# Performance work log

Hardware: AMD Instinct MI355X
Metric: run time of the kernel (lower is better)

## Reference

```python
import jax, jax.numpy as jnp
import numpy as np

N = 50000
E = 400000
IN_FEATS = 256
HIDDEN = 64
HEADS = 8
CLASSES = 40
NEG_SLOPE = 0.2  # DGL GATConv default negative_slope


def setup_inputs() -> dict:
    key = jax.random.key(0)
    ks = jax.random.split(key, 12)
    features = jax.random.normal(ks[0], (N, IN_FEATS), dtype=jnp.float32)
    src = jax.random.randint(ks[1], (E,), 0, N, dtype=jnp.int32)
    dst = jax.random.randint(ks[2], (E,), 0, N, dtype=jnp.int32)
    s = 0.05
    # layer 0: in_feats -> HEADS*HIDDEN
    W1 = jax.random.normal(ks[3], (IN_FEATS, HEADS * HIDDEN), dtype=jnp.float32) * s
    al1 = jax.random.normal(ks[4], (HEADS, HIDDEN), dtype=jnp.float32) * s
    ar1 = jax.random.normal(ks[5], (HEADS, HIDDEN), dtype=jnp.float32) * s
    # layer 1: HEADS*HIDDEN -> HEADS*HIDDEN
    W2 = jax.random.normal(ks[6], (HEADS * HIDDEN, HEADS * HIDDEN), dtype=jnp.float32) * s
    al2 = jax.random.normal(ks[7], (HEADS, HIDDEN), dtype=jnp.float32) * s
    ar2 = jax.random.normal(ks[8], (HEADS, HIDDEN), dtype=jnp.float32) * s
    # layer 2: HEADS*HIDDEN -> 1*CLASSES
    W3 = jax.random.normal(ks[9], (HEADS * HIDDEN, CLASSES), dtype=jnp.float32) * s
    al3 = jax.random.normal(ks[10], (1, CLASSES), dtype=jnp.float32) * s
    ar3 = jax.random.normal(ks[11], (1, CLASSES), dtype=jnp.float32) * s
    return {"features": features, "src": src, "dst": dst,
            "W1": W1, "al1": al1, "ar1": ar1,
            "W2": W2, "al2": al2, "ar2": ar2,
            "W3": W3, "al3": al3, "ar3": ar3}


def gat_conv(h, W, al, ar, src, dst):
    """DGL GATConv (no bias, no residual, no activation, no dropout)."""
    H, D = al.shape
    feat = (h @ W).reshape(N, H, D)                      # [N,H,D]
    el = jnp.sum(feat * al[None], axis=-1)               # [N,H]
    er = jnp.sum(feat * ar[None], axis=-1)               # [N,H]
    e = jax.nn.leaky_relu(el[src] + er[dst], NEG_SLOPE)  # [E,H]
    # edge softmax over incoming edges of each dst node
    m = jax.ops.segment_max(e, dst, num_segments=N)      # [N,H]
    ex = jnp.exp(e - m[dst])                             # [E,H]
    denom = jax.ops.segment_sum(ex, dst, num_segments=N) # [N,H]
    alpha = ex / denom[dst]                              # [E,H]
    msg = alpha[:, :, None] * feat[src]                  # [E,H,D]
    out = jax.ops.segment_sum(msg, dst, num_segments=N)  # [N,H,D]
    return out.reshape(N, H * D)


def reference(features, src, dst, W1, al1, ar1, W2, al2, ar2, W3, al3, ar3):
    h = gat_conv(features, W1, al1, ar1, src, dst)  # [N, HEADS*HIDDEN]
    h = gat_conv(h, W2, al2, ar2, src, dst)         # [N, HEADS*HIDDEN]
    h = gat_conv(h, W3, al3, ar3, src, dst)         # [N, CLASSES]
    return h
```

## Files before the change

### kernel.cpp

```cpp
#include <hip/hip_runtime.h>
#include <hip/hip_bf16.h>

#define NN 50000
#define NE 400000
#define MPAD 50048
#define SLOTS 48

typedef __bf16 bf16x8_t __attribute__((ext_vector_type(8)));
typedef __bf16 bf16x4_t __attribute__((ext_vector_type(4)));
typedef float f32x4_t __attribute__((ext_vector_type(4)));

__device__ __forceinline__ float bhi(unsigned int u) {
    union { unsigned int i; float f; } v; v.i = u & 0xffff0000u; return v.f;
}
__device__ __forceinline__ float blo(unsigned int u) {
    union { unsigned int i; float f; } v; v.i = u << 16; return v.f;
}

__global__ __launch_bounds__(256) void prep_kernel(
    const float* __restrict__ W1, __hip_bfloat16* __restrict__ W1t,
    const float* __restrict__ W2, __hip_bfloat16* __restrict__ W2t,
    const float* __restrict__ W3, __hip_bfloat16* __restrict__ W3t,
    const float* __restrict__ al1, const float* __restrict__ ar1,
    const float* __restrict__ al2, const float* __restrict__ ar2,
    __hip_bfloat16* __restrict__ walr1, __hip_bfloat16* __restrict__ walr2) {
    int stride = gridDim.x * blockDim.x;
    for (int i = blockIdx.x * blockDim.x + threadIdx.x; i < 512 * 512; i += stride) {
        if (i < 512 * 256) {
            int n = i >> 8, k = i & 255;
            W1t[i] = __float2bfloat16(W1[k * 512 + n]);
        }
        {
            int n = i >> 9, k = i & 511;
            W2t[i] = __float2bfloat16(W2[k * 512 + n]);
        }
        if (i < 48 * 512) {
            int n = i >> 9, k = i & 511;
            W3t[i] = __float2bfloat16((n < 40) ? W3[k * 40 + n] : 0.f);
        }
        if (i < 16 * 256) {
            int j = i >> 8, k = i & 255;
            const float* v = (j < 8) ? (al1 + j * 64) : (ar1 + (j - 8) * 64);
            float s = 0.f;
            for (int d = 0; d < 64; ++d) s += W1[(size_t)k * 512 + (j & 7) * 64 + d] * v[d];
            walr1[(k >> 5) * 512 + j * 32 + (k & 31)] = __float2bfloat16(s);
        }
        if (i < 16 * 512) {
            int j = i >> 9, k = i & 511;
            const float* v = (j < 8) ? (al2 + j * 64) : (ar2 + (j - 8) * 64);
            float s = 0.f;
            for (int d = 0; d < 64; ++d) s += W2[(size_t)k * 512 + (j & 7) * 64 + d] * v[d];
            walr2[(k >> 5) * 512 + j * 32 + (k & 31)] = __float2bfloat16(s);
        }
    }
}

__global__ void build_kernel(const int* __restrict__ src, const int* __restrict__ dst,
                             int* __restrict__ deg, int* __restrict__ slot) {
    int e = blockIdx.x * blockDim.x + threadIdx.x;
    if (e < NE) {
        int d = dst[e];
        int p = atomicAdd(&deg[d], 1);
        if (p < SLOTS) slot[(size_t)d * SLOTS + p] = src[e];
    }
}

__device__ __forceinline__ void gld_lds16(const void* g, void* l) {
    __builtin_amdgcn_global_load_lds(
        (const __attribute__((address_space(1))) unsigned int*)g,
        (__attribute__((address_space(3))) unsigned int*)l, 16, 0, 0);
}

__global__ __launch_bounds__(256) void gemm1_fused(const float* __restrict__ A,
                                                   const __hip_bfloat16* __restrict__ Wt,
                                                   const __hip_bfloat16* __restrict__ walr,
                                                   __hip_bfloat16* __restrict__ C,
                                                   float* __restrict__ el,
                                                   float* __restrict__ er) {
    const int K = 256;
    __shared__ __align__(16) char smem[16384];
    char* smemA = smem;
    char* smemB = smem + 8192;
    const int row0 = blockIdx.x * 128;
    const int col0 = blockIdx.y * 128;
    const int w = threadIdx.x >> 6;
    const int lane = threadIdx.x & 63;
    const int quad = lane >> 4, l15 = lane & 15;
    const int wm = (w >> 1) * 64, wn = (w & 1) * 64;
    const int c0 = w * 2;
    const int srow = lane >> 2;
    const int skel = (lane & 3) * 8;
    const bool my_e = (blockIdx.y == 0) && ((w & 1) == 0);

    f32x4_t acc[4][4] = {};
    f32x4_t acce[4] = {};
    for (int k0 = 0; k0 < K; k0 += 32) {
        __syncthreads();
        {
#pragma unroll
            for (int cc = 0; cc < 2; ++cc) {
                int row = row0 + (c0 + cc) * 16 + srow;
                int rc = (row < NN) ? row : (NN - 1);
                const float* p = A + (size_t)rc * K + k0 + skel;
                float4 f0 = *reinterpret_cast<const float4*>(p);
                float4 f1 = *reinterpret_cast<const float4*>(p + 4);
                bf16x8_t h;
                h[0] = (__bf16)f0.x; h[1] = (__bf16)f0.y;
                h[2] = (__bf16)f0.z; h[3] = (__bf16)f0.w;
                h[4] = (__bf16)f1.x; h[5] = (__bf16)f1.y;
                h[6] = (__bf16)f1.z; h[7] = (__bf16)f1.w;
                *reinterpret_cast<bf16x8_t*>(smemA + (c0 + cc) * 1024 + srow * 64 +
                                             (lane & 3) * 16) = h;
            }
            const __hip_bfloat16* gB0 = Wt + (size_t)(col0 + c0 * 16 + srow) * K + k0 + skel;
            gld_lds16(gB0, smemB + c0 * 1024);
            gld_lds16(gB0 + (size_t)16 * K, smemB + (c0 + 1) * 1024);
        }
        __syncthreads();
        bf16x8_t a[4], b[4];
#pragma unroll
        for (int mi = 0; mi < 4; mi++)
            a[mi] = *reinterpret_cast<const bf16x8_t*>(smemA + (wm + mi * 16 + l15) * 64 + quad * 16);
#pragma unroll
        for (int ni = 0; ni < 4; ni++)
            b[ni] = *reinterpret_cast<const bf16x8_t*>(smemB + (wn + ni * 16 + l15) * 64 + quad * 16);
#pragma unroll
        for (int mi = 0; mi < 4; mi++)
#pragma unroll
            for (int ni = 0; ni < 4; ni++)
                acc[mi][ni] = __builtin_amdgcn_mfma_f32_16x16x32_bf16(a[mi], b[ni], acc[mi][ni], 0, 0, 0);
        if (my_e) {
            bf16x8_t b5 = *reinterpret_cast<const bf16x8_t*>(
                walr + (k0 >> 5) * 512 + l15 * 32 + quad * 8);
#pragma unroll
            for (int mi = 0; mi < 4; mi++)
                acce[mi] = __builtin_amdgcn_mfma_f32_16x16x32_bf16(a[mi], b5, acce[mi], 0, 0, 0);
        }
    }
#pragma unroll
    for (int mi = 0; mi < 4; mi++) {
#pragma unroll
        for (int ni = 0; ni < 4; ni++) {
#pragma unroll
            for (int r = 0; r < 4; r++) {
                int row = row0 + wm + mi * 16 + quad * 4 + r;
                if (row < NN)
                    C[(size_t)row * 512 + col0 + wn + ni * 16 + l15] =
                        __float2bfloat16(acc[mi][ni][r]);
            }
        }
    }
    if (my_e) {
#pragma unroll
        for (int mi = 0; mi < 4; mi++) {
#pragma unroll
            for (int r = 0; r < 4; r++) {
                int row = row0 + wm + mi * 16 + quad * 4 + r;
                if (row < NN) {
                    float v = acce[mi][r];
                    if (l15 < 8) el[row * 8 + l15] = v;
                    else er[row * 8 + l15 - 8] = v;
                }
            }
        }
    }
}

__global__ __launch_bounds__(256) void gemm_bt_fused(const __hip_bfloat16* __restrict__ A,
                                                     const __hip_bfloat16* __restrict__ Wt,
                                                     const __hip_bfloat16* __restrict__ walr,
                                                     __hip_bfloat16* __restrict__ C,
                                                     float* __restrict__ el,
                                                     float* __restrict__ er) {
    const int K = 512;
    __shared__ __align__(16) char smem[16384];
    char* smemA = smem;
    char* smemB = smem + 8192;
    const int row0 = blockIdx.x * 128;
    const int col0 = blockIdx.y * 128;
    const int w = threadIdx.x >> 6;
    const int lane = threadIdx.x & 63;
    const int quad = lane >> 4, l15 = lane & 15;
    const int wm = (w >> 1) * 64, wn = (w & 1) * 64;
    const int c0 = w * 2;
    const int srow = lane >> 2;
    const int skel = (lane & 3) * 8;
    const bool my_e = (blockIdx.y == 0) && ((w & 1) == 0);

    f32x4_t acc[4][4] = {};
    f32x4_t acce[4] = {};
    for (int k0 = 0; k0 < K; k0 += 32) {
        __syncthreads();
        {
            const __hip_bfloat16* gA0 = A + (size_t)(row0 + c0 * 16 + srow) * K + k0 + skel;
            const __hip_bfloat16* gB0 = Wt + (size_t)(col0 + c0 * 16 + srow) * K + k0 + skel;
            gld_lds16(gA0, smemA + c0 * 1024);
            gld_lds16(gA0 + (size_t)16 * K, smemA + (c0 + 1) * 1024);
            gld_lds16(gB0, smemB + c0 * 1024);
            gld_lds16(gB0 + (size_t)16 * K, smemB + (c0 + 1) * 1024);
        }
        __syncthreads();
        bf16x8_t a[4], b[4];
#pragma unroll
        for (int mi = 0; mi < 4; mi++)
            a[mi] = *reinterpret_cast<const bf16x8_t*>(smemA + (wm + mi * 16 + l15) * 64 + quad * 16);
#pragma unroll
        for (int ni = 0; ni < 4; ni++)
            b[ni] = *reinterpret_cast<const bf16x8_t*>(smemB + (wn + ni * 16 + l15) * 64 + quad * 16);
#pragma unroll
        for (int mi = 0; mi < 4; mi++)
#pragma unroll
            for (int ni = 0; ni < 4; ni++)
                acc[mi][ni] = __builtin_amdgcn_mfma_f32_16x16x32_bf16(a[mi], b[ni], acc[mi][ni], 0, 0, 0);
        if (my_e) {
            bf16x8_t b5 = *reinterpret_cast<const bf16x8_t*>(
                walr + (k0 >> 5) * 512 + l15 * 32 + quad * 8);
#pragma unroll
            for (int mi = 0; mi < 4; mi++)
                acce[mi] = __builtin_amdgcn_mfma_f32_16x16x32_bf16(a[mi], b5, acce[mi], 0, 0, 0);
        }
    }
#pragma unroll
    for (int mi = 0; mi < 4; mi++) {
#pragma unroll
        for (int ni = 0; ni < 4; ni++) {
#pragma unroll
            for (int r = 0; r < 4; r++) {
                int row = row0 + wm + mi * 16 + quad * 4 + r;
                if (row < NN)
                    C[(size_t)row * 512 + col0 + wn + ni * 16 + l15] =
                        __float2bfloat16(acc[mi][ni][r]);
            }
        }
    }
    if (my_e) {
#pragma unroll
        for (int mi = 0; mi < 4; mi++) {
#pragma unroll
            for (int r = 0; r < 4; r++) {
                int row = row0 + wm + mi * 16 + quad * 4 + r;
                if (row < NN) {
                    float v = acce[mi][r];
                    if (l15 < 8) el[row * 8 + l15] = v;
                    else er[row * 8 + l15 - 8] = v;
                }
            }
        }
    }
}

#define W3_LDSROW 520
__global__ __launch_bounds__(256) void gemm3_mfma(const __hip_bfloat16* __restrict__ A,
                                                  const __hip_bfloat16* __restrict__ W3t,
                                                  const float* __restrict__ al,
                                                  const float* __restrict__ ar,
                                                  __hip_bfloat16* __restrict__ C,
                                                  float* __restrict__ el,
                                                  float* __restrict__ er) {
    __shared__ __align__(16) __hip_bfloat16 wlds[48 * W3_LDSROW];
    for (int c = threadIdx.x; c < 48 * 64; c += 256) {
        int n = c >> 6, koff = (c & 63) * 8;
        *reinterpret_cast<uint4*>(&wlds[n * W3_LDSROW + koff]) =
            *reinterpret_cast<const uint4*>(W3t + n * 512 + koff);
    }
    __syncthreads();
    const int w = threadIdx.x >> 6;
    const int lane = threadIdx.x & 63;
    const int quad = lane >> 4, l15 = lane & 15;
    const int row0 = blockIdx.x * 64 + w * 16;

    float alv[3], arv[3];
#pragma unroll
    for (int c = 0; c < 3; c++) {
        int col = c * 16 + l15;
        alv[c] = (col < 40) ? al[col] : 0.f;
        arv[c] = (col < 40) ? ar[col] : 0.f;
    }

    f32x4_t acc[3] = {};
    const __hip_bfloat16* arow = A + (size_t)(row0 + l15) * 512;
#pragma unroll 4
    for (int k0 = 0; k0 < 512; k0 += 32) {
        bf16x8_t a = *reinterpret_cast<const bf16x8_t*>(arow + k0 + quad * 8);
#pragma unroll
        for (int c = 0; c < 3; c++) {
            bf16x8_t b = *reinterpret_cast<const bf16x8_t*>(
                &wlds[(c * 16 + l15) * W3_LDSROW + k0 + quad * 8]);
            acc[c] = __builtin_amdgcn_mfma_f32_16x16x32_bf16(a, b, acc[c], 0, 0, 0);
        }
    }
#pragma unroll
    for (int r = 0; r < 4; r++) {
        int row = row0 + quad * 4 + r;
        bool rok = row < NN;
        float pl = 0.f, pr = 0.f;
#pragma unroll
        for (int c = 0; c < 3; c++) {
            float v = acc[c][r];
            if (rok) C[(size_t)row * 64 + c * 16 + l15] = __float2bfloat16(v);
            pl += v * alv[c];
            pr += v * arv[c];
        }
        if (rok) C[(size_t)row * 64 + 48 + l15] = __float2bfloat16(0.f);
        pl += __shfl_xor(pl, 1, 64); pr += __shfl_xor(pr, 1, 64);
        pl += __shfl_xor(pl, 2, 64); pr += __shfl_xor(pr, 2, 64);
        pl += __shfl_xor(pl, 4, 64); pr += __shfl_xor(pr, 4, 64);
        pl += __shfl_xor(pl, 8, 64); pr += __shfl_xor(pr, 8, 64);
        if (l15 == 0 && rok) { el[row] = pl; er[row] = pr; }
    }
}

__device__ __forceinline__ void fma8(float* acc, float pj, const uint4& q) {
    acc[0] += pj * blo(q.x); acc[1] += pj * bhi(q.x);
    acc[2] += pj * blo(q.y); acc[3] += pj * bhi(q.y);
    acc[4] += pj * blo(q.z); acc[5] += pj * bhi(q.z);
    acc[6] += pj * blo(q.w); acc[7] += pj * bhi(q.w);
}

__global__ __launch_bounds__(256) void agg8_kernel(const __hip_bfloat16* __restrict__ feat,
                                                   const float* __restrict__ el,
                                                   const float* __restrict__ er,
                                                   const int* __restrict__ deg,
                                                   const int* __restrict__ slot,
                                                   __hip_bfloat16* __restrict__ out) {
    int n = (blockIdx.x * blockDim.x + threadIdx.x) >> 6;
    int lane = threadIdx.x & 63;
    if (n >= NN) return;
    const int es = lane >> 3;
    const int h8 = lane & 7;
    const int hd = lane >> 3;
    int dn = min(deg[n], SLOTS);
    float er_n = er[n * 8 + h8];
    const int* sl = slot + (size_t)n * SLOTS;

    float lsum = 0.f;
    float acc[8] = {};
    for (int base = 0; base < dn; base += 8) {
        int e = base + es;
        bool valid = e < dn;
        int s = valid ? sl[e] : 0;
        float t = el[s * 8 + h8] + er_n;
        float x = (t >= 0.f) ? t : 0.2f * t;
        float p = valid ? __expf(x) : 0.f;
        lsum += p;
        int cnt = min(8, dn - base);
        int j = 0;
        for (; j + 4 <= cnt; j += 4) {
            int s0 = __builtin_amdgcn_readlane(s, (j + 0) * 8);
            int s1 = __builtin_amdgcn_readlane(s, (j + 1) * 8);
            int s2 = __builtin_amdgcn_readlane(s, (j + 2) * 8);
            int s3 = __builtin_amdgcn_readlane(s, (j + 3) * 8);
            float p0 = __shfl(p, (j + 0) * 8 + hd, 64);
            float p1 = __shfl(p, (j + 1) * 8 + hd, 64);
            float p2 = __shfl(p, (j + 2) * 8 + hd, 64);
            float p3 = __shfl(p, (j + 3) * 8 + hd, 64);
            uint4 q0 = *reinterpret_cast<const uint4*>(feat + (size_t)s0 * 512 + lane * 8);
            uint4 q1 = *reinterpret_cast<const uint4*>(feat + (size_t)s1 * 512 + lane * 8);
            uint4 q2 = *reinterpret_cast<const uint4*>(feat + (size_t)s2 * 512 + lane * 8);
            uint4 q3 = *reinterpret_cast<const uint4*>(feat + (size_t)s3 * 512 + lane * 8);
            fma8(acc, p0, q0);
            fma8(acc, p1, q1);
            fma8(acc, p2, q2);
            fma8(acc, p3, q3);
        }
        for (; j < cnt; ++j) {
            int sj = __builtin_amdgcn_readlane(s, j * 8);
            float pj = __shfl(p, j * 8 + hd, 64);
            uint4 q = *reinterpret_cast<const uint4*>(feat + (size_t)sj * 512 + lane * 8);
            fma8(acc, pj, q);
        }
    }
    lsum += __shfl_xor(lsum, 8, 64);
    lsum += __shfl_xor(lsum, 16, 64);
    lsum += __shfl_xor(lsum, 32, 64);
    float lh = __shfl(lsum, hd, 64);
    float inv = (lh > 0.f) ? 1.f / lh : 0.f;
    bf16x8_t o8;
#pragma unroll
    for (int d = 0; d < 8; ++d) o8[d] = (__bf16)(acc[d] * inv);
    *reinterpret_cast<bf16x8_t*>(out + (size_t)n * 512 + lane * 8) = o8;
}

__global__ __launch_bounds__(256) void agg3_kernel(const __hip_bfloat16* __restrict__ feat,
                                                   const float* __restrict__ el,
                                                   const float* __restrict__ er,
                                                   const int* __restrict__ deg,
                                                   const int* __restrict__ slot,
                                                   float* __restrict__ out) {
    int n = (blockIdx.x * blockDim.x + threadIdx.x) >> 6;
    int lane = threadIdx.x & 63;
    if (n >= NN) return;
    const int es = lane >> 3;
    const int dc = lane & 7;
    int dn = min(deg[n], SLOTS);
    float er_n = er[n];
    const int* sl = slot + (size_t)n * SLOTS;

    float lsum = 0.f;
    float acc[8] = {};
    for (int base = 0; base < dn; base += 16) {
        int e0 = base + es, e1 = base + 8 + es;
        bool v0 = e0 < dn, v1 = e1 < dn;
        int s0 = v0 ? sl[e0] : 0;
        int s1 = v1 ? sl[e1] : 0;
        float t0 = el[s0] + er_n;
        float t1 = el[s1] + er_n;
        float x0 = (t0 >= 0.f) ? t0 : 0.2f * t0;
        float x1 = (t1 >= 0.f) ? t1 : 0.2f * t1;
        float p0 = v0 ? __expf(x0) : 0.f;
        float p1 = v1 ? __expf(x1) : 0.f;
        lsum += p0 + p1;
        uint4 q0 = *reinterpret_cast<const uint4*>(feat + (size_t)s0 * 64 + dc * 8);
        uint4 q1 = *reinterpret_cast<const uint4*>(feat + (size_t)s1 * 64 + dc * 8);
        acc[0] += p0 * blo(q0.x) + p1 * blo(q1.x);
        acc[1] += p0 * bhi(q0.x) + p1 * bhi(q1.x);
        acc[2] += p0 * blo(q0.y) + p1 * blo(q1.y);
        acc[3] += p0 * bhi(q0.y) + p1 * bhi(q1.y);
        acc[4] += p0 * blo(q0.z) + p1 * blo(q1.z);
        acc[5] += p0 * bhi(q0.z) + p1 * bhi(q1.z);
        acc[6] += p0 * blo(q0.w) + p1 * blo(q1.w);
        acc[7] += p0 * bhi(q0.w) + p1 * bhi(q1.w);
    }
    lsum += __shfl_xor(lsum, 8, 64);
    lsum += __shfl_xor(lsum, 16, 64);
    lsum += __shfl_xor(lsum, 32, 64);
#pragma unroll
    for (int d = 0; d < 8; ++d) {
        acc[d] += __shfl_xor(acc[d], 8, 64);
        acc[d] += __shfl_xor(acc[d], 16, 64);
        acc[d] += __shfl_xor(acc[d], 32, 64);
    }
    float inv = (lsum > 0.f) ? 1.f / lsum : 0.f;
    if (es == 0 && dc < 5) {
        float4 o0 = make_float4(acc[0] * inv, acc[1] * inv, acc[2] * inv, acc[3] * inv);
        float4 o1 = make_float4(acc[4] * inv, acc[5] * inv, acc[6] * inv, acc[7] * inv);
        *reinterpret_cast<float4*>(out + (size_t)n * 40 + dc * 8) = o0;
        *reinterpret_cast<float4*>(out + (size_t)n * 40 + dc * 8 + 4) = o1;
    }
}

extern "C" void kernel_launch(void* const* d_in, const int* in_sizes, int n_in,
                              void* d_out, int out_size, void* d_ws, size_t ws_size,
                              hipStream_t stream) {
    const float* features = (const float*)d_in[0];
    const int* src = (const int*)d_in[1];
    const int* dst = (const int*)d_in[2];
    const float* W1 = (const float*)d_in[3];
    const float* al1 = (const float*)d_in[4];
    const float* ar1 = (const float*)d_in[5];
    const float* W2 = (const float*)d_in[6];
    const float* al2 = (const float*)d_in[7];
    const float* ar2 = (const float*)d_in[8];
    const float* W3 = (const float*)d_in[9];
    const float* al3 = (const float*)d_in[10];
    const float* ar3 = (const float*)d_in[11];

    char* ws = (char*)d_ws;
    size_t o = 0;
    auto carve = [&](size_t bytes) -> void* {
        o = (o + 255) & ~(size_t)255;
        void* p = ws + o;
        o += bytes;
        return p;
    };
    __hip_bfloat16* Fbf = (__hip_bfloat16*)carve((size_t)MPAD * 512 * 2);
    __hip_bfloat16* Gbf = (__hip_bfloat16*)carve((size_t)MPAD * 512 * 2);
    __hip_bfloat16* W1t = (__hip_bfloat16*)carve((size_t)512 * 256 * 2);
    __hip_bfloat16* W2t = (__hip_bfloat16*)carve((size_t)512 * 512 * 2);
    __hip_bfloat16* W3t = (__hip_bfloat16*)carve((size_t)48 * 512 * 2);
    __hip_bfloat16* walr1 = (__hip_bfloat16*)carve((size_t)16 * 256 * 2);
    __hip_bfloat16* walr2 = (__hip_bfloat16*)carve((size_t)16 * 512 * 2);
    float* el = (float*)carve((size_t)NN * 8 * 4);
    float* er = (float*)carve((size_t)NN * 8 * 4);
    float* el3 = (float*)carve((size_t)NN * 4);
    float* er3 = (float*)carve((size_t)NN * 4);
    int* deg = (int*)carve((size_t)NN * 4);
    int* slot = (int*)carve((size_t)NN * SLOTS * 4);

    hipMemsetAsync(deg, 0, (size_t)NN * 4, stream);
    build_kernel<<<(NE + 255) / 256, 256, 0, stream>>>(src, dst, deg, slot);
    prep_kernel<<<512, 256, 0, stream>>>(W1, W1t, W2, W2t, W3, W3t,
                                         al1, ar1, al2, ar2, walr1, walr2);

    const int gmm = MPAD / 128;
    gemm1_fused<<<dim3(gmm, 4), 256, 0, stream>>>(features, W1t, walr1, Fbf, el, er);
    agg8_kernel<<<(NN + 3) / 4, 256, 0, stream>>>(Fbf, el, er, deg, slot, Gbf);
    gemm_bt_fused<<<dim3(gmm, 4), 256, 0, stream>>>(Gbf, W2t, walr2, Fbf, el, er);
    agg8_kernel<<<(NN + 3) / 4, 256, 0, stream>>>(Fbf, el, er, deg, slot, Gbf);
    gemm3_mfma<<<MPAD / 64, 256, 0, stream>>>(Gbf, W3t, al3, ar3, Fbf, el3, er3);
    agg3_kernel<<<(NN + 3) / 4, 256, 0, stream>>>(Fbf, el3, er3, deg, slot, (float*)d_out);
}
```

Baseline: 425.1 us.

## Double-buffer LDS in fused GEMMs and swap grid axes for tile reuse

Both fused GEMM kernels now use two LDS buffers and prefetch the next K-slice (global→LDS for bf16, registers for the fp32 A in gemm1) while computing the current one, with explicit vmcnt waits and raw barriers instead of two __syncthreads per step. The grid is also transposed so the four column blocks of the same row tile are adjacent in launch order, improving L2 reuse of A. This doubles LDS use to 32 KB per block and relies on hand-counted vmcnt values being correct.

```diff
diff --git a/kernel.cpp b/kernel.cpp
--- a/kernel.cpp
+++ b/kernel.cpp
@@ -78,11 +78,10 @@
                                                    float* __restrict__ el,
                                                    float* __restrict__ er) {
     const int K = 256;
-    __shared__ __align__(16) char smem[16384];
-    char* smemA = smem;
-    char* smemB = smem + 8192;
-    const int row0 = blockIdx.x * 128;
-    const int col0 = blockIdx.y * 128;
+    const int NT = K / 32;
+    __shared__ __align__(16) char smem[32768];
+    const int row0 = blockIdx.y * 128;
+    const int col0 = blockIdx.x * 128;
     const int w = threadIdx.x >> 6;
     const int lane = threadIdx.x & 63;
     const int quad = lane >> 4, l15 = lane & 15;
@@ -90,40 +89,76 @@
     const int c0 = w * 2;
     const int srow = lane >> 2;
     const int skel = (lane & 3) * 8;
-    const bool my_e = (blockIdx.y == 0) && ((w & 1) == 0);
+    const bool my_e = (blockIdx.x == 0) && ((w & 1) == 0);
+
+    const float* pA[2];
+#pragma unroll
+    for (int cc = 0; cc < 2; ++cc) {
+        int row = row0 + (c0 + cc) * 16 + srow;
+        int rc = (row < NN) ? row : (NN - 1);
+        pA[cc] = A + (size_t)rc * K + skel;
+    }
+    const __hip_bfloat16* gB = Wt + (size_t)(col0 + c0 * 16 + srow) * K + skel;
+
+    float4 frA[2][2];
+    float4 frB[2][2];
 
     f32x4_t acc[4][4] = {};
     f32x4_t acce[4] = {};
-    for (int k0 = 0; k0 < K; k0 += 32) {
-        __syncthreads();
-        {
+
+#pragma unroll
+    for (int cc = 0; cc < 2; ++cc) {
+        frA[cc][0] = *reinterpret_cast<const float4*>(pA[cc] + 0);
+        frA[cc][1] = *reinterpret_cast<const float4*>(pA[cc] + 4);
+    }
+    gld_lds16(gB + 0, smem + 8192 + c0 * 1024);
+    gld_lds16(gB + (size_t)16 * K, smem + 8192 + (c0 + 1) * 1024);
+
+#pragma unroll
+    for (int t = 0; t < NT; ++t) {
+        const int cur = t & 1, nxt = cur ^ 1;
+        char* sA = smem + cur * 16384;
+        char* sB = sA + 8192;
+        if (t + 1 < NT) {
+            const int k1 = (t + 1) * 32;
+            char* sBn = smem + nxt * 16384 + 8192;
 #pragma unroll
             for (int cc = 0; cc < 2; ++cc) {
-                int row = row0 + (c0 + cc) * 16 + srow;
-                int rc = (row < NN) ? row : (NN - 1);
-                const float* p = A + (size_t)rc * K + k0 + skel;
-                float4 f0 = *reinterpret_cast<const float4*>(p);
-                float4 f1 = *reinterpret_cast<const float4*>(p + 4);
-                bf16x8_t h;
-                h[0] = (__bf16)f0.x; h[1] = (__bf16)f0.y;
-                h[2] = (__bf16)f0.z; h[3] = (__bf16)f0.w;
-                h[4] = (__bf16)f1.x; h[5] = (__bf16)f1.y;
-                h[6] = (__bf16)f1.z; h[7] = (__bf16)f1.w;
-                *reinterpret_cast<bf16x8_t*>(smemA + (c0 + cc) * 1024 + srow * 64 +
-                                             (lane & 3) * 16) = h;
+                frB[cc][0] = *reinterpret_cast<const float4*>(pA[cc] + k1);
+                frB[cc][1] = *reinterpret_cast<const float4*>(pA[cc] + k1 + 4);
             }
-            const __hip_bfloat16* gB0 = Wt + (size_t)(col0 + c0 * 16 + srow) * K + k0 + skel;
-            gld_lds16(gB0, smemB + c0 * 1024);
-            gld_lds16(gB0 + (size_t)16 * K, smemB + (c0 + 1) * 1024);
-        }
-        __syncthreads();
+            gld_lds16(gB + k1, sBn + c0 * 1024);
+            gld_lds16(gB + k1 + (size_t)16 * K, sBn + (c0 + 1) * 1024);
+            asm volatile("s_waitcnt vmcnt(6)" ::: "memory");
+        } else {
+            asm volatile("s_waitcnt vmcnt(0)" ::: "memory");
+        }
+#pragma unroll
+        for (int cc = 0; cc < 2; ++cc) {
+            float4 f0 = frA[cc][0], f1 = frA[cc][1];
+            bf16x8_t h;
+            h[0] = (__bf16)f0.x; h[1] = (__bf16)f0.y;
+            h[2] = (__bf16)f0.z; h[3] = (__bf16)f0.w;
+            h[4] = (__bf16)f1.x; h[5] = (__bf16)f1.y;
+            h[6] = (__bf16)f1.z; h[7] = (__bf16)f1.w;
+            *reinterpret_cast<bf16x8_t*>(sA + (c0 + cc) * 1024 + srow * 64 +
+                                         (lane & 3) * 16) = h;
+        }
+#pragma unroll
+        for (int cc = 0; cc < 2; ++cc) {
+            frA[cc][0] = frB[cc][0];
+            frA[cc][1] = frB[cc][1];
+        }
+        asm volatile("s_waitcnt lgkmcnt(0)" ::: "memory");
+        __builtin_amdgcn_s_barrier();
+        asm volatile("" ::: "memory");
         bf16x8_t a[4], b[4];
 #pragma unroll
         for (int mi = 0; mi < 4; mi++)
-            a[mi] = *reinterpret_cast<const bf16x8_t*>(smemA + (wm + mi * 16 + l15) * 64 + quad * 16);
+            a[mi] = *reinterpret_cast<const bf16x8_t*>(sA + (wm + mi * 16 + l15) * 64 + quad * 16);
 #pragma unroll
         for (int ni = 0; ni < 4; ni++)
-            b[ni] = *reinterpret_cast<const bf16x8_t*>(smemB + (wn + ni * 16 + l15) * 64 + quad * 16);
+            b[ni] = *reinterpret_cast<const bf16x8_t*>(sB + (wn + ni * 16 + l15) * 64 + quad * 16);
 #pragma unroll
         for (int mi = 0; mi < 4; mi++)
 #pragma unroll
@@ -131,11 +166,14 @@
                 acc[mi][ni] = __builtin_amdgcn_mfma_f32_16x16x32_bf16(a[mi], b[ni], acc[mi][ni], 0, 0, 0);
         if (my_e) {
             bf16x8_t b5 = *reinterpret_cast<const bf16x8_t*>(
-                walr + (k0 >> 5) * 512 + l15 * 32 + quad * 8);
+                walr + t * 512 + l15 * 32 + quad * 8);
 #pragma unroll
             for (int mi = 0; mi < 4; mi++)
                 acce[mi] = __builtin_amdgcn_mfma_f32_16x16x32_bf16(a[mi], b5, acce[mi], 0, 0, 0);
         }
+        asm volatile("" ::: "memory");
+        __builtin_amdgcn_s_barrier();
+        asm volatile("" ::: "memory");
     }
 #pragma unroll
     for (int mi = 0; mi < 4; mi++) {
@@ -173,11 +211,10 @@
                                                      float* __restrict__ el,
                                                      float* __restrict__ er) {
     const int K = 512;
-    __shared__ __align__(16) char smem[16384];
-    char* smemA = smem;
-    char* smemB = smem + 8192;
-    const int row0 = blockIdx.x * 128;
-    const int col0 = blockIdx.y * 128;
+    const int NT = K / 32;
+    __shared__ __align__(16) char smem[32768];
+    const int row0 = blockIdx.y * 128;
+    const int col0 = blockIdx.x * 128;
     const int w = threadIdx.x >> 6;
     const int lane = threadIdx.x & 63;
     const int quad = lane >> 4, l15 = lane & 15;
@@ -185,28 +222,49 @@
     const int c0 = w * 2;
     const int srow = lane >> 2;
     const int skel = (lane & 3) * 8;
-    const bool my_e = (blockIdx.y == 0) && ((w & 1) == 0);
+    const bool my_e = (blockIdx.x == 0) && ((w & 1) == 0);
+
+    const __hip_bfloat16* gA = A + (size_t)(row0 + c0 * 16 + srow) * K + skel;
+    const __hip_bfloat16* gB = Wt + (size_t)(col0 + c0 * 16 + srow) * K + skel;
 
     f32x4_t acc[4][4] = {};
     f32x4_t acce[4] = {};
-    for (int k0 = 0; k0 < K; k0 += 32) {
-        __syncthreads();
-        {
-            const __hip_bfloat16* gA0 = A + (size_t)(row0 + c0 * 16 + srow) * K + k0 + skel;
-            const __hip_bfloat16* gB0 = Wt + (size_t)(col0 + c0 * 16 + srow) * K + k0 + skel;
-            gld_lds16(gA0, smemA + c0 * 1024);
-            gld_lds16(gA0 + (size_t)16 * K, smemA + (c0 + 1) * 1024);
-            gld_lds16(gB0, smemB + c0 * 1024);
-            gld_lds16(gB0 + (size_t)16 * K, smemB + (c0 + 1) * 1024);
-        }
-        __syncthreads();
+
+    {
+        char* sA = smem;
+        char* sB = smem + 8192;
+        gld_lds16(gA, sA + c0 * 1024);
+        gld_lds16(gA + (size_t)16 * K, sA + (c0 + 1) * 1024);
+        gld_lds16(gB, sB + c0 * 1024);
+        gld_lds16(gB + (size_t)16 * K, sB + (c0 + 1) * 1024);
+    }
+
+#pragma unroll
+    for (int t = 0; t < NT; ++t) {
+        const int cur = t & 1, nxt = cur ^ 1;
+        char* sA = smem + cur * 16384;
+        char* sB = sA + 8192;
+        if (t + 1 < NT) {
+            const int k1 = (t + 1) * 32;
+            char* sAn = smem + nxt * 16384;
+            char* sBn = sAn + 8192;
+            gld_lds16(gA + k1, sAn + c0 * 1024);
+            gld_lds16(gA + k1 + (size_t)16 * K, sAn + (c0 + 1) * 1024);
+            gld_lds16(gB + k1, sBn + c0 * 1024);
+            gld_lds16(gB + k1 + (size_t)16 * K, sBn + (c0 + 1) * 1024);
+            asm volatile("s_waitcnt vmcnt(4)" ::: "memory");
+        } else {
+            asm volatile("s_waitcnt vmcnt(0)" ::: "memory");
+        }
+        __builtin_amdgcn_s_barrier();
+        asm volatile("" ::: "memory");
         bf16x8_t a[4], b[4];
 #pragma unroll
         for (int mi = 0; mi < 4; mi++)
-            a[mi] = *reinterpret_cast<const bf16x8_t*>(smemA + (wm + mi * 16 + l15) * 64 + quad * 16);
+            a[mi] = *reinterpret_cast<const bf16x8_t*>(sA + (wm + mi * 16 + l15) * 64 + quad * 16);
 #pragma unroll
         for (int ni = 0; ni < 4; ni++)
-            b[ni] = *reinterpret_cast<const bf16x8_t*>(smemB + (wn + ni * 16 + l15) * 64 + quad * 16);
+            b[ni] = *reinterpret_cast<const bf16x8_t*>(sB + (wn + ni * 16 + l15) * 64 + quad * 16);
 #pragma unroll
         for (int mi = 0; mi < 4; mi++)
 #pragma unroll
@@ -214,11 +272,14 @@
                 acc[mi][ni] = __builtin_amdgcn_mfma_f32_16x16x32_bf16(a[mi], b[ni], acc[mi][ni], 0, 0, 0);
         if (my_e) {
             bf16x8_t b5 = *reinterpret_cast<const bf16x8_t*>(
-                walr + (k0 >> 5) * 512 + l15 * 32 + quad * 8);
+                walr + t * 512 + l15 * 32 + quad * 8);
 #pragma unroll
             for (int mi = 0; mi < 4; mi++)
                 acce[mi] = __builtin_amdgcn_mfma_f32_16x16x32_bf16(a[mi], b5, acce[mi], 0, 0, 0);
         }
+        asm volatile("" ::: "memory");
+        __builtin_amdgcn_s_barrier();
+        asm volatile("" ::: "memory");
     }
 #pragma unroll
     for (int mi = 0; mi < 4; mi++) {
@@ -483,9 +544,9 @@
                                          al1, ar1, al2, ar2, walr1, walr2);
 
     const int gmm = MPAD / 128;
-    gemm1_fused<<<dim3(gmm, 4), 256, 0, stream>>>(features, W1t, walr1, Fbf, el, er);
+    gemm1_fused<<<dim3(4, gmm), 256, 0, stream>>>(features, W1t, walr1, Fbf, el, er);
     agg8_kernel<<<(NN + 3) / 4, 256, 0, stream>>>(Fbf, el, er, deg, slot, Gbf);
-    gemm_bt_fused<<<dim3(gmm, 4), 256, 0, stream>>>(Gbf, W2t, walr2, Fbf, el, er);
+    gemm_bt_fused<<<dim3(4, gmm), 256, 0, stream>>>(Gbf, W2t, walr2, Fbf, el, er);
     agg8_kernel<<<(NN + 3) / 4, 256, 0, stream>>>(Fbf, el, er, deg, slot, Gbf);
     gemm3_mfma<<<MPAD / 64, 256, 0, stream>>>(Gbf, W3t, al3, ar3, Fbf, el3, er3);
     agg3_kernel<<<(NN + 3) / 4, 256, 0, stream>>>(Fbf, el3, er3, deg, slot, (float*)d_out);
```

After: 423.8 us. No clear change (-0.3%).

## Restructure GEMMs into full-width row tiles with double-buffered swizzled LDS

Applied to the files above, without the earlier changes.

Replaces the two layer GEMM kernels with a single templated kernel in which each block computes 64 rows across all 512 output columns. Each wave owns 128 columns, so the A tile is loaded once per block rather than once per column block. The kernel double-buffers A and B tiles in LDS using direct global-to-LDS loads with explicit vmcnt waits, and XOR-swizzles the LDS layout to reduce bank conflicts. The first layer's inline fp32-to-bf16 conversion moves into a separate cast kernel. The trade-offs are large LDS use (about 72KB per block), more accumulator registers per wave, re-reading the whole W tile in every block, and an extra pass over the features.

```diff
diff --git a/kernel.cpp b/kernel.cpp
--- a/kernel.cpp
+++ b/kernel.cpp
@@ -65,180 +65,117 @@
     }
 }
 
+__global__ __launch_bounds__(256) void cast_kernel(const float* __restrict__ f,
+                                                   __hip_bfloat16* __restrict__ o) {
+    int i = blockIdx.x * 256 + threadIdx.x;
+    const float* p = f + (size_t)i * 8;
+    float4 a = *reinterpret_cast<const float4*>(p);
+    float4 b = *reinterpret_cast<const float4*>(p + 4);
+    bf16x8_t h;
+    h[0] = (__bf16)a.x; h[1] = (__bf16)a.y; h[2] = (__bf16)a.z; h[3] = (__bf16)a.w;
+    h[4] = (__bf16)b.x; h[5] = (__bf16)b.y; h[6] = (__bf16)b.z; h[7] = (__bf16)b.w;
+    *reinterpret_cast<bf16x8_t*>(o + (size_t)i * 8) = h;
+}
+
 __device__ __forceinline__ void gld_lds16(const void* g, void* l) {
     __builtin_amdgcn_global_load_lds(
         (const __attribute__((address_space(1))) unsigned int*)g,
         (__attribute__((address_space(3))) unsigned int*)l, 16, 0, 0);
 }
 
-__global__ __launch_bounds__(256) void gemm1_fused(const float* __restrict__ A,
+template <int K>
+__global__ __launch_bounds__(256, 2) void gemm_all(const __hip_bfloat16* __restrict__ A,
                                                    const __hip_bfloat16* __restrict__ Wt,
                                                    const __hip_bfloat16* __restrict__ walr,
                                                    __hip_bfloat16* __restrict__ C,
                                                    float* __restrict__ el,
                                                    float* __restrict__ er) {
-    const int K = 256;
-    __shared__ __align__(16) char smem[16384];
-    char* smemA = smem;
-    char* smemB = smem + 8192;
-    const int row0 = blockIdx.x * 128;
-    const int col0 = blockIdx.y * 128;
+    const int NT = K / 32;
+    __shared__ __align__(16) char smem[2 * 36864];
     const int w = threadIdx.x >> 6;
     const int lane = threadIdx.x & 63;
     const int quad = lane >> 4, l15 = lane & 15;
-    const int wm = (w >> 1) * 64, wn = (w & 1) * 64;
-    const int c0 = w * 2;
+    const int row0 = blockIdx.x * 64;
     const int srow = lane >> 2;
-    const int skel = (lane & 3) * 8;
-    const bool my_e = (blockIdx.y == 0) && ((w & 1) == 0);
-
-    f32x4_t acc[4][4] = {};
+    const int csrc = ((lane & 3) ^ ((lane >> 3) & 3)) * 8;
+    const int rswz = l15 * 64 + ((quad ^ ((l15 >> 1) & 3)) << 4);
+
+    const __hip_bfloat16* gA = A + (size_t)(row0 + w * 16 + srow) * K + csrc;
+    const __hip_bfloat16* gBb = Wt + (size_t)(w * 128 + srow) * K + csrc;
+
+    f32x4_t acc[4][8] = {};
     f32x4_t acce[4] = {};
-    for (int k0 = 0; k0 < K; k0 += 32) {
-        __syncthreads();
-        {
-#pragma unroll
-            for (int cc = 0; cc < 2; ++cc) {
-                int row = row0 + (c0 + cc) * 16 + srow;
-                int rc = (row < NN) ? row : (NN - 1);
-                const float* p = A + (size_t)rc * K + k0 + skel;
-                float4 f0 = *reinterpret_cast<const float4*>(p);
-                float4 f1 = *reinterpret_cast<const float4*>(p + 4);
-                bf16x8_t h;
-                h[0] = (__bf16)f0.x; h[1] = (__bf16)f0.y;
-                h[2] = (__bf16)f0.z; h[3] = (__bf16)f0.w;
-                h[4] = (__bf16)f1.x; h[5] = (__bf16)f1.y;
-                h[6] = (__bf16)f1.z; h[7] = (__bf16)f1.w;
-                *reinterpret_cast<bf16x8_t*>(smemA + (c0 + cc) * 1024 + srow * 64 +
-                                             (lane & 3) * 16) = h;
-            }
-            const __hip_bfloat16* gB0 = Wt + (size_t)(col0 + c0 * 16 + srow) * K + k0 + skel;
-            gld_lds16(gB0, smemB + c0 * 1024);
-            gld_lds16(gB0 + (size_t)16 * K, smemB + (c0 + 1) * 1024);
-        }
-        __syncthreads();
-        bf16x8_t a[4], b[4];
+
+    {
+        char* buf = smem;
+        gld_lds16(gA, buf + w * 1024);
+#pragma unroll
+        for (int o = 0; o < 8; ++o)
+            gld_lds16(gBb + (size_t)o * 16 * K, buf + 4096 + (w * 8 + o) * 1024);
+    }
+
+#pragma unroll
+    for (int t = 0; t < NT; ++t) {
+        char* buf = smem + (t & 1) * 36864;
+        bf16x8_t b5;
+        if (w == 0) {
+            b5 = *reinterpret_cast<const bf16x8_t*>(walr + t * 512 + l15 * 32 + quad * 8);
+            asm volatile("" ::: "memory");
+        }
+        if (t + 1 < NT) {
+            char* nb = smem + ((t + 1) & 1) * 36864;
+            const int k1 = (t + 1) * 32;
+            gld_lds16(gA + k1, nb + w * 1024);
+#pragma unroll
+            for (int o = 0; o < 8; ++o)
+                gld_lds16(gBb + (size_t)o * 16 * K + k1, nb + 4096 + (w * 8 + o) * 1024);
+            asm volatile("s_waitcnt vmcnt(9)" ::: "memory");
+        } else {
+            asm volatile("s_waitcnt vmcnt(0)" ::: "memory");
+        }
+        __builtin_amdgcn_s_barrier();
+        asm volatile("" ::: "memory");
+        bf16x8_t a[4], b[8];
 #pragma unroll
         for (int mi = 0; mi < 4; mi++)
-            a[mi] = *reinterpret_cast<const bf16x8_t*>(smemA + (wm + mi * 16 + l15) * 64 + quad * 16);
-#pragma unroll
-        for (int ni = 0; ni < 4; ni++)
-            b[ni] = *reinterpret_cast<const bf16x8_t*>(smemB + (wn + ni * 16 + l15) * 64 + quad * 16);
+            a[mi] = *reinterpret_cast<const bf16x8_t*>(buf + mi * 1024 + rswz);
+#pragma unroll
+        for (int ni = 0; ni < 8; ni++)
+            b[ni] = *reinterpret_cast<const bf16x8_t*>(buf + 4096 + (w * 8 + ni) * 1024 + rswz);
 #pragma unroll
         for (int mi = 0; mi < 4; mi++)
 #pragma unroll
-            for (int ni = 0; ni < 4; ni++)
+            for (int ni = 0; ni < 8; ni++)
                 acc[mi][ni] = __builtin_amdgcn_mfma_f32_16x16x32_bf16(a[mi], b[ni], acc[mi][ni], 0, 0, 0);
-        if (my_e) {
-            bf16x8_t b5 = *reinterpret_cast<const bf16x8_t*>(
-                walr + (k0 >> 5) * 512 + l15 * 32 + quad * 8);
+        if (w == 0) {
 #pragma unroll
             for (int mi = 0; mi < 4; mi++)
                 acce[mi] = __builtin_amdgcn_mfma_f32_16x16x32_bf16(a[mi], b5, acce[mi], 0, 0, 0);
         }
-    }
+        asm volatile("" ::: "memory");
+        __builtin_amdgcn_s_barrier();
+        asm volatile("" ::: "memory");
+    }
+
 #pragma unroll
     for (int mi = 0; mi < 4; mi++) {
 #pragma unroll
-        for (int ni = 0; ni < 4; ni++) {
+        for (int ni = 0; ni < 8; ni++) {
 #pragma unroll
             for (int r = 0; r < 4; r++) {
-                int row = row0 + wm + mi * 16 + quad * 4 + r;
+                int row = row0 + mi * 16 + quad * 4 + r;
                 if (row < NN)
-                    C[(size_t)row * 512 + col0 + wn + ni * 16 + l15] =
+                    C[(size_t)row * 512 + w * 128 + ni * 16 + l15] =
                         __float2bfloat16(acc[mi][ni][r]);
             }
         }
     }
-    if (my_e) {
+    if (w == 0) {
 #pragma unroll
         for (int mi = 0; mi < 4; mi++) {
 #pragma unroll
             for (int r = 0; r < 4; r++) {
-                int row = row0 + wm + mi * 16 + quad * 4 + r;
-                if (row < NN) {
-                    float v = acce[mi][r];
-                    if (l15 < 8) el[row * 8 + l15] = v;
-                    else er[row * 8 + l15 - 8] = v;
-                }
-            }
-        }
-    }
-}
-
-__global__ __launch_bounds__(256) void gemm_bt_fused(const __hip_bfloat16* __restrict__ A,
-                                                     const __hip_bfloat16* __restrict__ Wt,
-                                                     const __hip_bfloat16* __restrict__ walr,
-                                                     __hip_bfloat16* __restrict__ C,
-                                                     float* __restrict__ el,
-                                                     float* __restrict__ er) {
-    const int K = 512;
-    __shared__ __align__(16) char smem[16384];
-    char* smemA = smem;
-    char* smemB = smem + 8192;
-    const int row0 = blockIdx.x * 128;
-    const int col0 = blockIdx.y * 128;
-    const int w = threadIdx.x >> 6;
-    const int lane = threadIdx.x & 63;
-    const int quad = lane >> 4, l15 = lane & 15;
-    const int wm = (w >> 1) * 64, wn = (w & 1) * 64;
-    const int c0 = w * 2;
-    const int srow = lane >> 2;
-    const int skel = (lane & 3) * 8;
-    const bool my_e = (blockIdx.y == 0) && ((w & 1) == 0);
-
-    f32x4_t acc[4][4] = {};
-    f32x4_t acce[4] = {};
-    for (int k0 = 0; k0 < K; k0 += 32) {
-        __syncthreads();
-        {
-            const __hip_bfloat16* gA0 = A + (size_t)(row0 + c0 * 16 + srow) * K + k0 + skel;
-            const __hip_bfloat16* gB0 = Wt + (size_t)(col0 + c0 * 16 + srow) * K + k0 + skel;
-            gld_lds16(gA0, smemA + c0 * 1024);
-            gld_lds16(gA0 + (size_t)16 * K, smemA + (c0 + 1) * 1024);
-            gld_lds16(gB0, smemB + c0 * 1024);
-            gld_lds16(gB0 + (size_t)16 * K, smemB + (c0 + 1) * 1024);
-        }
-        __syncthreads();
-        bf16x8_t a[4], b[4];
-#pragma unroll
-        for (int mi = 0; mi < 4; mi++)
-            a[mi] = *reinterpret_cast<const bf16x8_t*>(smemA + (wm + mi * 16 + l15) * 64 + quad * 16);
-#pragma unroll
-        for (int ni = 0; ni < 4; ni++)
-            b[ni] = *reinterpret_cast<const bf16x8_t*>(smemB + (wn + ni * 16 + l15) * 64 + quad * 16);
-#pragma unroll
-        for (int mi = 0; mi < 4; mi++)
-#pragma unroll
-            for (int ni = 0; ni < 4; ni++)
-                acc[mi][ni] = __builtin_amdgcn_mfma_f32_16x16x32_bf16(a[mi], b[ni], acc[mi][ni], 0, 0, 0);
-        if (my_e) {
-            bf16x8_t b5 = *reinterpret_cast<const bf16x8_t*>(
-                walr + (k0 >> 5) * 512 + l15 * 32 + quad * 8);
-#pragma unroll
-            for (int mi = 0; mi < 4; mi++)
-                acce[mi] = __builtin_amdgcn_mfma_f32_16x16x32_bf16(a[mi], b5, acce[mi], 0, 0, 0);
-        }
-    }
-#pragma unroll
-    for (int mi = 0; mi < 4; mi++) {
-#pragma unroll
-        for (int ni = 0; ni < 4; ni++) {
-#pragma unroll
-            for (int r = 0; r < 4; r++) {
-                int row = row0 + wm + mi * 16 + quad * 4 + r;
-                if (row < NN)
-                    C[(size_t)row * 512 + col0 + wn + ni * 16 + l15] =
-                        __float2bfloat16(acc[mi][ni][r]);
-            }
-        }
-    }
-    if (my_e) {
-#pragma unroll
-        for (int mi = 0; mi < 4; mi++) {
-#pragma unroll
-            for (int r = 0; r < 4; r++) {
-                int row = row0 + wm + mi * 16 + quad * 4 + r;
+                int row = row0 + mi * 16 + quad * 4 + r;
                 if (row < NN) {
                     float v = acce[mi][r];
                     if (l15 < 8) el[row * 8 + l15] = v;
@@ -482,10 +419,11 @@
     prep_kernel<<<512, 256, 0, stream>>>(W1, W1t, W2, W2t, W3, W3t,
                                          al1, ar1, al2, ar2, walr1, walr2);
 
-    const int gmm = MPAD / 128;
-    gemm1_fused<<<dim3(gmm, 4), 256, 0, stream>>>(features, W1t, walr1, Fbf, el, er);
+    const int gmm = MPAD / 64;
+    cast_kernel<<<(NN * 256 / 8) / 256, 256, 0, stream>>>(features, Gbf);
+    gemm_all<256><<<gmm, 256, 0, stream>>>(Gbf, W1t, walr1, Fbf, el, er);
     agg8_kernel<<<(NN + 3) / 4, 256, 0, stream>>>(Fbf, el, er, deg, slot, Gbf);
-    gemm_bt_fused<<<dim3(gmm, 4), 256, 0, stream>>>(Gbf, W2t, walr2, Fbf, el, er);
+    gemm_all<512><<<gmm, 256, 0, stream>>>(Gbf, W2t, walr2, Fbf, el, er);
     agg8_kernel<<<(NN + 3) / 4, 256, 0, stream>>>(Fbf, el, er, deg, slot, Gbf);
     gemm3_mfma<<<MPAD / 64, 256, 0, stream>>>(Gbf, W3t, al3, ar3, Fbf, el3, er3);
     agg3_kernel<<<(NN + 3) / 4, 256, 0, stream>>>(Fbf, el3, er3, deg, slot, (float*)d_out);
```

New measurement: 398.9 us (median of 2 runs). -6.2%, faster.
